# Optimization experiments

Measured on AMD Instinct MI355X. Metric: run time of the kernel, lower is better.

Reference implementation:

```python
import jax, jax.numpy as jnp
import numpy as np

TEMPERATURE = 0.5
EPS = 1e-8  # torch CosineSimilarity eps


def setup_inputs() -> dict:
    key = jax.random.key(0)
    k1, k2 = jax.random.split(key)
    N, D = 4096, 256
    z1 = jax.random.normal(k1, (N, D), dtype=jnp.float32)
    z2 = jax.random.normal(k2, (N, D), dtype=jnp.float32)
    return {"z1": z1, "z2": z2}


def reference(z1, z2):
    N = z1.shape[0]
    z = jnp.concatenate([z1, z2], axis=0)  # [2N, D]
    # cosine similarity = normalized dot products (GEMM instead of O(N^2 D) broadcast)
    norm = jnp.linalg.norm(z, axis=-1, keepdims=True)
    zn = z / jnp.maximum(norm, EPS)
    sim = (zn @ zn.T) / TEMPERATURE  # [2N, 2N]
    # mask self-similarity on the diagonal
    idx = jnp.arange(2 * N)
    sim = jnp.where(idx[:, None] == idx[None, :], -jnp.inf, sim)
    # target[i] = (i - N) mod 2N  (arange(2N).roll(N))
    target = jnp.roll(idx, N)
    logp = jax.nn.log_softmax(sim, axis=-1)
    loss = -jnp.mean(logp[idx, target])
    return loss
```

## Files before the change

kernel.cpp:

```cpp
#include <hip/hip_runtime.h>

typedef __bf16 bf16x8 __attribute__((ext_vector_type(8)));
typedef float f32x4 __attribute__((ext_vector_type(4)));

#define TWO_LOG2E 2.88539008177792681f

#define GLOADLDS16(g, l) __builtin_amdgcn_global_load_lds(                     \
    (const __attribute__((address_space(1))) void*)(g),                        \
    (__attribute__((address_space(3))) void*)(l), 16, 0, 0)

__device__ __forceinline__ unsigned f2bf(float f) {
    unsigned u = __float_as_uint(f);
    return (u + 0x7FFFu + ((u >> 16) & 1u)) >> 16;
}

__global__ void __launch_bounds__(256) normalize_kernel(
    const float* __restrict__ z1, const float* __restrict__ z2,
    unsigned short* __restrict__ zn, float* __restrict__ S, float* __restrict__ out)
{
    if (blockIdx.x < 32) S[(blockIdx.x << 8) + threadIdx.x] = 0.f;
    if (blockIdx.x == 32 && threadIdx.x == 0) out[0] = 0.f;

    const int wave = threadIdx.x >> 6, lane = threadIdx.x & 63;
    const int row = (blockIdx.x << 2) + wave;
    const float* src = (row < 4096) ? (z1 + row * 256) : (z2 + (row - 4096) * 256);
    float4 v = ((const float4*)src)[lane];
    float ss = v.x * v.x + v.y * v.y + v.z * v.z + v.w * v.w;
#pragma unroll
    for (int m = 32; m > 0; m >>= 1) ss += __shfl_xor(ss, m, 64);
    float sc = 1.0f / fmaxf(sqrtf(ss), 1e-8f);
    uint2 w;
    w.x = f2bf(v.x * sc) | (f2bf(v.y * sc) << 16);
    w.y = f2bf(v.z * sc) | (f2bf(v.w * sc) << 16);
    *(uint2*)(zn + row * 256 + (lane << 2)) = w;
}

__global__ void __launch_bounds__(512, 4) simexp_kernel(
    const unsigned short* __restrict__ zn, float* __restrict__ S)
{
    __shared__ __align__(16) unsigned short Bs[4][2048];

    const int tid = threadIdx.x;
    const int wv = tid >> 6, lane = tid & 63;
    const int q = lane >> 4, n16 = lane & 15;
    const int g = wv >> 2, wl = wv & 3;

    int ti, tj, nrep = 1;
    {
        int job = blockIdx.x;
        if (job < 496) {
            int t = 0, rem = job;
            while (rem >= 31 - t) { rem -= 31 - t; ++t; }
            ti = t; tj = t + 1 + rem;
        } else {
            ti = tj = (job - 496) << 1;
            nrep = 2;
        }
    }

    for (int rep = 0; rep < nrep; ++rep) {
        const int rT = ti + rep, cT = tj + rep;
        const bool diag = (rT == cT);
        const int colTile = cT << 8;
        const int rowW = (rT << 8) + (wv << 5);

        bf16x8 a[2][8];
#pragma unroll
        for (int rt = 0; rt < 2; ++rt)
#pragma unroll
            for (int ks = 0; ks < 8; ++ks)
                a[rt][ks] = *(const bf16x8*)(zn + ((rowW + (rt << 4) + n16) << 8)
                                                + (ks << 5) + (q << 3));

        auto stage = [&](int m) {
            const int colBase = colTile + ((m >> 2) << 5);
            const int koff = (m & 3) << 6;
            unsigned short* base = &Bs[m & 3][0];
            int s = (wl << 6) + lane;
            int c = s >> 3, d = s & 7;
            int k8 = d ^ (c & 7);
            GLOADLDS16(zn + ((colBase + c) << 8) + koff + (k8 << 3), base + (s << 3));
        };

        float rs[2][4];
#pragma unroll
        for (int i = 0; i < 2; ++i)
#pragma unroll
            for (int j = 0; j < 4; ++j) rs[i][j] = 0.f;

        f32x4 acc[2][2];
        auto consume = [&](int kc) {
            const unsigned short* bb = &Bs[kc & 3][0];
#pragma unroll
            for (int ks = 0; ks < 2; ++ks) {
                bf16x8 bf[2];
#pragma unroll
                for (int ct = 0; ct < 2; ++ct) {
                    int c  = (ct << 4) + n16;
                    int k8 = ((ks << 2) + q) ^ (c & 7);
                    bf[ct] = *(const bf16x8*)(bb + (((c << 3) + k8) << 3));
                }
#pragma unroll
                for (int rt = 0; rt < 2; ++rt)
#pragma unroll
                    for (int ct = 0; ct < 2; ++ct)
                        acc[rt][ct] = __builtin_amdgcn_mfma_f32_16x16x32_bf16(
                            a[rt][(kc << 1) + ks], bf[ct], acc[rt][ct], 0, 0, 0);
            }
        };
        auto zacc = [&]() {
#pragma unroll
            for (int rt = 0; rt < 2; ++rt)
#pragma unroll
                for (int ct = 0; ct < 2; ++ct) acc[rt][ct] = (f32x4){0.f, 0.f, 0.f, 0.f};
        };
        auto epiRC = [&](bool doCol, int ccc) {
            float cs[2] = {0.f, 0.f};
#pragma unroll
            for (int rt = 0; rt < 2; ++rt)
#pragma unroll
                for (int ct = 0; ct < 2; ++ct)
#pragma unroll
                    for (int r = 0; r < 4; ++r) {
                        float e = __builtin_amdgcn_exp2f(acc[rt][ct][r] * TWO_LOG2E);
                        rs[rt][r] += e;
                        cs[ct] += e;
                    }
            if (doCol) {
#pragma unroll
                for (int ct = 0; ct < 2; ++ct) {
                    float s = cs[ct];
                    s += __shfl_xor(s, 16, 64);
                    s += __shfl_xor(s, 32, 64);
                    if (lane < 16)
                        atomicAdd(&S[colTile + (ccc << 5) + (ct << 4) + n16], s);
                }
            }
        };

        if (g == 0) stage(0); else stage(1);

        for (int cc = 0; cc < 7; ++cc) {
            zacc();
            const bool act   = !diag || (cc >= wv);
            const bool doCol = !diag || (cc >  wv);
#pragma unroll
            for (int kc = 0; kc < 4; ++kc) {
                if ((kc & 1) == g) {
                    stage((cc << 2) + kc + 2);
                    asm volatile("s_waitcnt vmcnt(1)" ::: "memory");
                }
                __builtin_amdgcn_s_barrier();
                asm volatile("" ::: "memory");
                if (act) consume(kc);
            }
            if (act) epiRC(doCol, cc);
        }
        zacc();
        if (g == 0) { stage(30); asm volatile("s_waitcnt vmcnt(1)" ::: "memory"); }
        __builtin_amdgcn_s_barrier();
        asm volatile("" ::: "memory");
        consume(0);
        if (g == 1) { stage(31); asm volatile("s_waitcnt vmcnt(1)" ::: "memory"); }
        __builtin_amdgcn_s_barrier();
        asm volatile("" ::: "memory");
        consume(1);
        if (g == 0) { asm volatile("s_waitcnt vmcnt(0)" ::: "memory"); }
        __builtin_amdgcn_s_barrier();
        asm volatile("" ::: "memory");
        consume(2);
        if (g == 1) { asm volatile("s_waitcnt vmcnt(0)" ::: "memory"); }
        __builtin_amdgcn_s_barrier();
        asm volatile("" ::: "memory");
        consume(3);
        epiRC(!diag || (wv < 7), 7);

#pragma unroll
        for (int rt = 0; rt < 2; ++rt)
#pragma unroll
            for (int r = 0; r < 4; ++r) {
                float s = rs[rt][r];
                s += __shfl_xor(s, 1, 64);
                s += __shfl_xor(s, 2, 64);
                s += __shfl_xor(s, 4, 64);
                s += __shfl_xor(s, 8, 64);
                if (n16 == 0) atomicAdd(&S[rowW + (rt << 4) + (q << 2) + r], s);
            }
    }
}

__global__ void __launch_bounds__(256) finish_kernel(
    const unsigned short* __restrict__ zn, const float* __restrict__ S,
    float* __restrict__ out)
{
    __shared__ float vals[16];
    const int tid = threadIdx.x, lane = tid & 63, wave = tid >> 6;
    const int q = lane >> 4, n16 = lane & 15;
    const int rib = (wave << 2) + q;
    const int row = (blockIdx.x << 4) + rib;
    const int tar = (row + 4096) & 8191;

    float drr = 0.f, drt = 0.f;
#pragma unroll
    for (int i = 0; i < 4; ++i) {
        int k = (i << 6) + (n16 << 2);
        uint2 ur = *(const uint2*)(zn + (row << 8) + k);
        uint2 ut = *(const uint2*)(zn + (tar << 8) + k);
        float a0 = __uint_as_float(ur.x << 16),  a1 = __uint_as_float(ur.x & 0xFFFF0000u);
        float a2 = __uint_as_float(ur.y << 16),  a3 = __uint_as_float(ur.y & 0xFFFF0000u);
        float b0 = __uint_as_float(ut.x << 16),  b1 = __uint_as_float(ut.x & 0xFFFF0000u);
        float b2 = __uint_as_float(ut.y << 16),  b3 = __uint_as_float(ut.y & 0xFFFF0000u);
        drr += a0 * a0 + a1 * a1 + a2 * a2 + a3 * a3;
        drt += a0 * b0 + a1 * b1 + a2 * b2 + a3 * b3;
    }
#pragma unroll
    for (int m = 1; m <= 8; m <<= 1) {
        drr += __shfl_xor(drr, m, 64);
        drt += __shfl_xor(drt, m, 64);
    }
    if (n16 == 0) {
        float Sv = S[row] - __builtin_amdgcn_exp2f(drr * TWO_LOG2E);
        vals[rib] = 0.693147180559945f * __builtin_amdgcn_logf(Sv) - 2.0f * drt;
    }
    __syncthreads();
    if (tid == 0) {
        float s = 0.f;
#pragma unroll
        for (int i = 0; i < 16; ++i) s += vals[i];
        atomicAdd(out, s * (1.0f / 8192.0f));
    }
}

extern "C" void kernel_launch(void* const* d_in, const int* in_sizes, int n_in,
                              void* d_out, int out_size, void* d_ws, size_t ws_size,
                              hipStream_t stream)
{
    const float* z1 = (const float*)d_in[0];
    const float* z2 = (const float*)d_in[1];
    unsigned short* zn = (unsigned short*)d_ws;
    float* S = (float*)((char*)d_ws + 8192 * 256 * sizeof(unsigned short));
    float* out = (float*)d_out;

    normalize_kernel<<<2048, 256, 0, stream>>>(z1, z2, zn, S, out);
    simexp_kernel<<<512, 512, 0, stream>>>(zn, S);
    finish_kernel<<<512, 256, 0, stream>>>(zn, S, out);
}
```

Baseline: 110.3 us.

## Split diagonal tile jobs into direct-load path; reduce column sums via LDS

Diagonal-tile blocks now take a separate path that skips the LDS-staged pipeline and barriers. Their waves read B fragments straight from global memory and loop only over the upper-triangular chunks. Waves are paired in mirrored order across the two reps so that per-wave work balances out. Off-diagonal blocks now write per-wave column partial sums into a shared buffer and do one atomic per column after a block sync, replacing per-wave global atomics. The costs are extra LDS, a block-wide sync, and uncached global B reads on the diagonal path.

```diff
diff --git a/kernel.cpp b/kernel.cpp
--- a/kernel.cpp
+++ b/kernel.cpp
@@ -39,153 +39,230 @@
     const unsigned short* __restrict__ zn, float* __restrict__ S)
 {
     __shared__ __align__(16) unsigned short Bs[4][2048];
+    __shared__ float colpart[8][256];
 
     const int tid = threadIdx.x;
     const int wv = tid >> 6, lane = tid & 63;
     const int q = lane >> 4, n16 = lane & 15;
     const int g = wv >> 2, wl = wv & 3;
-
-    int ti, tj, nrep = 1;
-    {
-        int job = blockIdx.x;
-        if (job < 496) {
-            int t = 0, rem = job;
-            while (rem >= 31 - t) { rem -= 31 - t; ++t; }
-            ti = t; tj = t + 1 + rem;
-        } else {
-            ti = tj = (job - 496) << 1;
-            nrep = 2;
-        }
-    }
-
-    for (int rep = 0; rep < nrep; ++rep) {
-        const int rT = ti + rep, cT = tj + rep;
-        const bool diag = (rT == cT);
-        const int colTile = cT << 8;
-        const int rowW = (rT << 8) + (wv << 5);
-
-        bf16x8 a[2][8];
-#pragma unroll
-        for (int rt = 0; rt < 2; ++rt)
-#pragma unroll
-            for (int ks = 0; ks < 8; ++ks)
-                a[rt][ks] = *(const bf16x8*)(zn + ((rowW + (rt << 4) + n16) << 8)
-                                                + (ks << 5) + (q << 3));
-
-        auto stage = [&](int m) {
-            const int colBase = colTile + ((m >> 2) << 5);
-            const int koff = (m & 3) << 6;
-            unsigned short* base = &Bs[m & 3][0];
-            int s = (wl << 6) + lane;
-            int c = s >> 3, d = s & 7;
-            int k8 = d ^ (c & 7);
-            GLOADLDS16(zn + ((colBase + c) << 8) + koff + (k8 << 3), base + (s << 3));
-        };
-
-        float rs[2][4];
-#pragma unroll
-        for (int i = 0; i < 2; ++i)
-#pragma unroll
-            for (int j = 0; j < 4; ++j) rs[i][j] = 0.f;
-
-        f32x4 acc[2][2];
-        auto consume = [&](int kc) {
-            const unsigned short* bb = &Bs[kc & 3][0];
-#pragma unroll
-            for (int ks = 0; ks < 2; ++ks) {
-                bf16x8 bf[2];
-#pragma unroll
-                for (int ct = 0; ct < 2; ++ct) {
-                    int c  = (ct << 4) + n16;
-                    int k8 = ((ks << 2) + q) ^ (c & 7);
-                    bf[ct] = *(const bf16x8*)(bb + (((c << 3) + k8) << 3));
-                }
+    const int job = blockIdx.x;
+
+    if (job >= 496) {
+        const int t0 = (job - 496) << 1;
+        for (int rep = 0; rep < 2; ++rep) {
+            const int t = t0 + rep;
+            const int wp = rep ? (7 - wv) : wv;
+            const int colTile = t << 8;
+            const int rowW = colTile + (wp << 5);
+
+            bf16x8 a[2][8];
+#pragma unroll
+            for (int rt = 0; rt < 2; ++rt)
+#pragma unroll
+                for (int ks = 0; ks < 8; ++ks)
+                    a[rt][ks] = *(const bf16x8*)(zn + ((rowW + (rt << 4) + n16) << 8)
+                                                    + (ks << 5) + (q << 3));
+            float rs[2][4];
+#pragma unroll
+            for (int i = 0; i < 2; ++i)
+#pragma unroll
+                for (int j = 0; j < 4; ++j) rs[i][j] = 0.f;
+
+            for (int cc = wp; cc < 8; ++cc) {
+                f32x4 acc[2][2];
 #pragma unroll
                 for (int rt = 0; rt < 2; ++rt)
 #pragma unroll
                     for (int ct = 0; ct < 2; ++ct)
-                        acc[rt][ct] = __builtin_amdgcn_mfma_f32_16x16x32_bf16(
-                            a[rt][(kc << 1) + ks], bf[ct], acc[rt][ct], 0, 0, 0);
-            }
-        };
-        auto zacc = [&]() {
-#pragma unroll
-            for (int rt = 0; rt < 2; ++rt)
-#pragma unroll
-                for (int ct = 0; ct < 2; ++ct) acc[rt][ct] = (f32x4){0.f, 0.f, 0.f, 0.f};
-        };
-        auto epiRC = [&](bool doCol, int ccc) {
-            float cs[2] = {0.f, 0.f};
-#pragma unroll
-            for (int rt = 0; rt < 2; ++rt)
-#pragma unroll
-                for (int ct = 0; ct < 2; ++ct)
-#pragma unroll
-                    for (int r = 0; r < 4; ++r) {
-                        float e = __builtin_amdgcn_exp2f(acc[rt][ct][r] * TWO_LOG2E);
-                        rs[rt][r] += e;
-                        cs[ct] += e;
+                        acc[rt][ct] = (f32x4){0.f, 0.f, 0.f, 0.f};
+#pragma unroll
+                for (int kc = 0; kc < 4; ++kc)
+#pragma unroll
+                    for (int ks = 0; ks < 2; ++ks) {
+                        bf16x8 bf[2];
+#pragma unroll
+                        for (int ct = 0; ct < 2; ++ct) {
+                            int col = colTile + (cc << 5) + (ct << 4) + n16;
+                            bf[ct] = *(const bf16x8*)(zn + (col << 8)
+                                        + (((kc << 1) + ks) << 5) + (q << 3));
+                        }
+#pragma unroll
+                        for (int rt = 0; rt < 2; ++rt)
+#pragma unroll
+                            for (int ct = 0; ct < 2; ++ct)
+                                acc[rt][ct] = __builtin_amdgcn_mfma_f32_16x16x32_bf16(
+                                    a[rt][(kc << 1) + ks], bf[ct], acc[rt][ct], 0, 0, 0);
                     }
-            if (doCol) {
-#pragma unroll
-                for (int ct = 0; ct < 2; ++ct) {
-                    float s = cs[ct];
-                    s += __shfl_xor(s, 16, 64);
-                    s += __shfl_xor(s, 32, 64);
-                    if (lane < 16)
-                        atomicAdd(&S[colTile + (ccc << 5) + (ct << 4) + n16], s);
+                float cs[2] = {0.f, 0.f};
+#pragma unroll
+                for (int rt = 0; rt < 2; ++rt)
+#pragma unroll
+                    for (int ct = 0; ct < 2; ++ct)
+#pragma unroll
+                        for (int r = 0; r < 4; ++r) {
+                            float e = __builtin_amdgcn_exp2f(acc[rt][ct][r] * TWO_LOG2E);
+                            rs[rt][r] += e;
+                            cs[ct] += e;
+                        }
+                if (cc > wp) {
+#pragma unroll
+                    for (int ct = 0; ct < 2; ++ct) {
+                        float s = cs[ct];
+                        s += __shfl_xor(s, 16, 64);
+                        s += __shfl_xor(s, 32, 64);
+                        if (lane < 16)
+                            atomicAdd(&S[colTile + (cc << 5) + (ct << 4) + n16], s);
+                    }
                 }
             }
-        };
-
-        if (g == 0) stage(0); else stage(1);
-
-        for (int cc = 0; cc < 7; ++cc) {
-            zacc();
-            const bool act   = !diag || (cc >= wv);
-            const bool doCol = !diag || (cc >  wv);
-#pragma unroll
-            for (int kc = 0; kc < 4; ++kc) {
-                if ((kc & 1) == g) {
-                    stage((cc << 2) + kc + 2);
-                    asm volatile("s_waitcnt vmcnt(1)" ::: "memory");
+#pragma unroll
+            for (int rt = 0; rt < 2; ++rt)
+#pragma unroll
+                for (int r = 0; r < 4; ++r) {
+                    float s = rs[rt][r];
+                    s += __shfl_xor(s, 1, 64);
+                    s += __shfl_xor(s, 2, 64);
+                    s += __shfl_xor(s, 4, 64);
+                    s += __shfl_xor(s, 8, 64);
+                    if (n16 == 0) atomicAdd(&S[rowW + (rt << 4) + (q << 2) + r], s);
                 }
-                __builtin_amdgcn_s_barrier();
-                asm volatile("" ::: "memory");
-                if (act) consume(kc);
+        }
+        return;
+    }
+
+    int ti, tj;
+    {
+        int t = 0, rem = job;
+        while (rem >= 31 - t) { rem -= 31 - t; ++t; }
+        ti = t; tj = t + 1 + rem;
+    }
+    const int colTile = tj << 8;
+    const int rowW = (ti << 8) + (wv << 5);
+
+    bf16x8 a[2][8];
+#pragma unroll
+    for (int rt = 0; rt < 2; ++rt)
+#pragma unroll
+        for (int ks = 0; ks < 8; ++ks)
+            a[rt][ks] = *(const bf16x8*)(zn + ((rowW + (rt << 4) + n16) << 8)
+                                            + (ks << 5) + (q << 3));
+
+    auto stage = [&](int m) {
+        const int colBase = colTile + ((m >> 2) << 5);
+        const int koff = (m & 3) << 6;
+        unsigned short* base = &Bs[m & 3][0];
+        int s = (wl << 6) + lane;
+        int c = s >> 3, d = s & 7;
+        int k8 = d ^ (c & 7);
+        GLOADLDS16(zn + ((colBase + c) << 8) + koff + (k8 << 3), base + (s << 3));
+    };
+
+    float rs[2][4];
+#pragma unroll
+    for (int i = 0; i < 2; ++i)
+#pragma unroll
+        for (int j = 0; j < 4; ++j) rs[i][j] = 0.f;
+
+    f32x4 acc[2][2];
+    auto consume = [&](int kc) {
+        const unsigned short* bb = &Bs[kc & 3][0];
+#pragma unroll
+        for (int ks = 0; ks < 2; ++ks) {
+            bf16x8 bf[2];
+#pragma unroll
+            for (int ct = 0; ct < 2; ++ct) {
+                int c  = (ct << 4) + n16;
+                int k8 = ((ks << 2) + q) ^ (c & 7);
+                bf[ct] = *(const bf16x8*)(bb + (((c << 3) + k8) << 3));
             }
-            if (act) epiRC(doCol, cc);
-        }
+#pragma unroll
+            for (int rt = 0; rt < 2; ++rt)
+#pragma unroll
+                for (int ct = 0; ct < 2; ++ct)
+                    acc[rt][ct] = __builtin_amdgcn_mfma_f32_16x16x32_bf16(
+                        a[rt][(kc << 1) + ks], bf[ct], acc[rt][ct], 0, 0, 0);
+        }
+    };
+    auto zacc = [&]() {
+#pragma unroll
+        for (int rt = 0; rt < 2; ++rt)
+#pragma unroll
+            for (int ct = 0; ct < 2; ++ct) acc[rt][ct] = (f32x4){0.f, 0.f, 0.f, 0.f};
+    };
+    auto epiC = [&](int cc) {
+        float cs[2] = {0.f, 0.f};
+#pragma unroll
+        for (int rt = 0; rt < 2; ++rt)
+#pragma unroll
+            for (int ct = 0; ct < 2; ++ct)
+#pragma unroll
+                for (int r = 0; r < 4; ++r) {
+                    float e = __builtin_amdgcn_exp2f(acc[rt][ct][r] * TWO_LOG2E);
+                    rs[rt][r] += e;
+                    cs[ct] += e;
+                }
+#pragma unroll
+        for (int ct = 0; ct < 2; ++ct) {
+            float s = cs[ct];
+            s += __shfl_xor(s, 16, 64);
+            s += __shfl_xor(s, 32, 64);
+            if (lane < 16) colpart[wv][(cc << 5) + (ct << 4) + n16] = s;
+        }
+    };
+
+    if (g == 0) stage(0); else stage(1);
+
+    for (int cc = 0; cc < 7; ++cc) {
         zacc();
-        if (g == 0) { stage(30); asm volatile("s_waitcnt vmcnt(1)" ::: "memory"); }
-        __builtin_amdgcn_s_barrier();
-        asm volatile("" ::: "memory");
-        consume(0);
-        if (g == 1) { stage(31); asm volatile("s_waitcnt vmcnt(1)" ::: "memory"); }
-        __builtin_amdgcn_s_barrier();
-        asm volatile("" ::: "memory");
-        consume(1);
-        if (g == 0) { asm volatile("s_waitcnt vmcnt(0)" ::: "memory"); }
-        __builtin_amdgcn_s_barrier();
-        asm volatile("" ::: "memory");
-        consume(2);
-        if (g == 1) { asm volatile("s_waitcnt vmcnt(0)" ::: "memory"); }
-        __builtin_amdgcn_s_barrier();
-        asm volatile("" ::: "memory");
-        consume(3);
-        epiRC(!diag || (wv < 7), 7);
-
-#pragma unroll
-        for (int rt = 0; rt < 2; ++rt)
-#pragma unroll
-            for (int r = 0; r < 4; ++r) {
-                float s = rs[rt][r];
-                s += __shfl_xor(s, 1, 64);
-                s += __shfl_xor(s, 2, 64);
-                s += __shfl_xor(s, 4, 64);
-                s += __shfl_xor(s, 8, 64);
-                if (n16 == 0) atomicAdd(&S[rowW + (rt << 4) + (q << 2) + r], s);
+#pragma unroll
+        for (int kc = 0; kc < 4; ++kc) {
+            if ((kc & 1) == g) {
+                stage((cc << 2) + kc + 2);
+                asm volatile("s_waitcnt vmcnt(1)" ::: "memory");
             }
+            __builtin_amdgcn_s_barrier();
+            asm volatile("" ::: "memory");
+            consume(kc);
+        }
+        epiC(cc);
+    }
+    zacc();
+    if (g == 0) { stage(30); asm volatile("s_waitcnt vmcnt(1)" ::: "memory"); }
+    __builtin_amdgcn_s_barrier();
+    asm volatile("" ::: "memory");
+    consume(0);
+    if (g == 1) { stage(31); asm volatile("s_waitcnt vmcnt(1)" ::: "memory"); }
+    __builtin_amdgcn_s_barrier();
+    asm volatile("" ::: "memory");
+    consume(1);
+    if (g == 0) { asm volatile("s_waitcnt vmcnt(0)" ::: "memory"); }
+    __builtin_amdgcn_s_barrier();
+    asm volatile("" ::: "memory");
+    consume(2);
+    if (g == 1) { asm volatile("s_waitcnt vmcnt(0)" ::: "memory"); }
+    __builtin_amdgcn_s_barrier();
+    asm volatile("" ::: "memory");
+    consume(3);
+    epiC(7);
+
+#pragma unroll
+    for (int rt = 0; rt < 2; ++rt)
+#pragma unroll
+        for (int r = 0; r < 4; ++r) {
+            float s = rs[rt][r];
+            s += __shfl_xor(s, 1, 64);
+            s += __shfl_xor(s, 2, 64);
+            s += __shfl_xor(s, 4, 64);
+            s += __shfl_xor(s, 8, 64);
+            if (n16 == 0) atomicAdd(&S[rowW + (rt << 4) + (q << 2) + r], s);
+        }
+
+    __syncthreads();
+    if (tid < 256) {
+        float s = 0.f;
+#pragma unroll
+        for (int w = 0; w < 8; ++w) s += colpart[w][tid];
+        atomicAdd(&S[colTile + tid], s);
     }
 }
 
```

New measurement: 117.6 us. 1.07x slower.

## Reduce column sums in LDS and give each diagonal tile its own block

Applied to the files above, without the earlier changes.

Column exp-sums for off-diagonal tiles are now written per wave into a shared-memory buffer and combined once per block. That replaces the per-wave global atomics issued after every column chunk with one atomic per column. Diagonal tiles are now handled one per block (528 blocks instead of 512) and compute the full tile for row sums only, dropping the triangular skip logic. This cuts global atomic traffic and branching, at the cost of 8KB extra LDS, a trailing block-wide sync, and redundant MFMA work on diagonal tiles.

```diff
diff --git a/kernel.cpp b/kernel.cpp
--- a/kernel.cpp
+++ b/kernel.cpp
@@ -39,153 +39,156 @@
     const unsigned short* __restrict__ zn, float* __restrict__ S)
 {
     __shared__ __align__(16) unsigned short Bs[4][2048];
+    __shared__ float colpart[8][256];
 
     const int tid = threadIdx.x;
     const int wv = tid >> 6, lane = tid & 63;
     const int q = lane >> 4, n16 = lane & 15;
     const int g = wv >> 2, wl = wv & 3;
-
-    int ti, tj, nrep = 1;
-    {
-        int job = blockIdx.x;
-        if (job < 496) {
-            int t = 0, rem = job;
-            while (rem >= 31 - t) { rem -= 31 - t; ++t; }
-            ti = t; tj = t + 1 + rem;
-        } else {
-            ti = tj = (job - 496) << 1;
-            nrep = 2;
-        }
-    }
-
-    for (int rep = 0; rep < nrep; ++rep) {
-        const int rT = ti + rep, cT = tj + rep;
-        const bool diag = (rT == cT);
-        const int colTile = cT << 8;
-        const int rowW = (rT << 8) + (wv << 5);
-
-        bf16x8 a[2][8];
+    const int job = blockIdx.x;
+
+    int ti, tj;
+    bool diag;
+    if (job >= 496) {
+        ti = tj = job - 496;
+        diag = true;
+    } else {
+        int t = 0, rem = job;
+        while (rem >= 31 - t) { rem -= 31 - t; ++t; }
+        ti = t; tj = t + 1 + rem;
+        diag = false;
+    }
+    const int colTile = tj << 8;
+    const int rowW = (ti << 8) + (wv << 5);
+
+    bf16x8 a[2][8];
+#pragma unroll
+    for (int rt = 0; rt < 2; ++rt)
+#pragma unroll
+        for (int ks = 0; ks < 8; ++ks)
+            a[rt][ks] = *(const bf16x8*)(zn + ((rowW + (rt << 4) + n16) << 8)
+                                            + (ks << 5) + (q << 3));
+
+    auto stage = [&](int m) {
+        const int colBase = colTile + ((m >> 2) << 5);
+        const int koff = (m & 3) << 6;
+        unsigned short* base = &Bs[m & 3][0];
+        int s = (wl << 6) + lane;
+        int c = s >> 3, d = s & 7;
+        int k8 = d ^ (c & 7);
+        GLOADLDS16(zn + ((colBase + c) << 8) + koff + (k8 << 3), base + (s << 3));
+    };
+
+    float rs[2][4];
+#pragma unroll
+    for (int i = 0; i < 2; ++i)
+#pragma unroll
+        for (int j = 0; j < 4; ++j) rs[i][j] = 0.f;
+
+    f32x4 acc[2][2];
+    auto consume = [&](int kc) {
+        const unsigned short* bb = &Bs[kc & 3][0];
+#pragma unroll
+        for (int ks = 0; ks < 2; ++ks) {
+            bf16x8 bf[2];
+#pragma unroll
+            for (int ct = 0; ct < 2; ++ct) {
+                int c  = (ct << 4) + n16;
+                int k8 = ((ks << 2) + q) ^ (c & 7);
+                bf[ct] = *(const bf16x8*)(bb + (((c << 3) + k8) << 3));
+            }
+#pragma unroll
+            for (int rt = 0; rt < 2; ++rt)
+#pragma unroll
+                for (int ct = 0; ct < 2; ++ct)
+                    acc[rt][ct] = __builtin_amdgcn_mfma_f32_16x16x32_bf16(
+                        a[rt][(kc << 1) + ks], bf[ct], acc[rt][ct], 0, 0, 0);
+        }
+    };
+    auto zacc = [&]() {
 #pragma unroll
         for (int rt = 0; rt < 2; ++rt)
 #pragma unroll
-            for (int ks = 0; ks < 8; ++ks)
-                a[rt][ks] = *(const bf16x8*)(zn + ((rowW + (rt << 4) + n16) << 8)
-                                                + (ks << 5) + (q << 3));
-
-        auto stage = [&](int m) {
-            const int colBase = colTile + ((m >> 2) << 5);
-            const int koff = (m & 3) << 6;
-            unsigned short* base = &Bs[m & 3][0];
-            int s = (wl << 6) + lane;
-            int c = s >> 3, d = s & 7;
-            int k8 = d ^ (c & 7);
-            GLOADLDS16(zn + ((colBase + c) << 8) + koff + (k8 << 3), base + (s << 3));
-        };
-
-        float rs[2][4];
-#pragma unroll
-        for (int i = 0; i < 2; ++i)
-#pragma unroll
-            for (int j = 0; j < 4; ++j) rs[i][j] = 0.f;
-
-        f32x4 acc[2][2];
-        auto consume = [&](int kc) {
-            const unsigned short* bb = &Bs[kc & 3][0];
-#pragma unroll
-            for (int ks = 0; ks < 2; ++ks) {
-                bf16x8 bf[2];
-#pragma unroll
-                for (int ct = 0; ct < 2; ++ct) {
-                    int c  = (ct << 4) + n16;
-                    int k8 = ((ks << 2) + q) ^ (c & 7);
-                    bf[ct] = *(const bf16x8*)(bb + (((c << 3) + k8) << 3));
+            for (int ct = 0; ct < 2; ++ct) acc[rt][ct] = (f32x4){0.f, 0.f, 0.f, 0.f};
+    };
+    auto epiC = [&](int cc) {
+        float cs[2] = {0.f, 0.f};
+#pragma unroll
+        for (int rt = 0; rt < 2; ++rt)
+#pragma unroll
+            for (int ct = 0; ct < 2; ++ct)
+#pragma unroll
+                for (int r = 0; r < 4; ++r) {
+                    float e = __builtin_amdgcn_exp2f(acc[rt][ct][r] * TWO_LOG2E);
+                    rs[rt][r] += e;
+                    cs[ct] += e;
                 }
-#pragma unroll
-                for (int rt = 0; rt < 2; ++rt)
-#pragma unroll
-                    for (int ct = 0; ct < 2; ++ct)
-                        acc[rt][ct] = __builtin_amdgcn_mfma_f32_16x16x32_bf16(
-                            a[rt][(kc << 1) + ks], bf[ct], acc[rt][ct], 0, 0, 0);
+        if (!diag) {
+#pragma unroll
+            for (int ct = 0; ct < 2; ++ct) {
+                float s = cs[ct];
+                s += __shfl_xor(s, 16, 64);
+                s += __shfl_xor(s, 32, 64);
+                if (lane < 16) colpart[wv][(cc << 5) + (ct << 4) + n16] = s;
             }
-        };
-        auto zacc = [&]() {
-#pragma unroll
-            for (int rt = 0; rt < 2; ++rt)
-#pragma unroll
-                for (int ct = 0; ct < 2; ++ct) acc[rt][ct] = (f32x4){0.f, 0.f, 0.f, 0.f};
-        };
-        auto epiRC = [&](bool doCol, int ccc) {
-            float cs[2] = {0.f, 0.f};
-#pragma unroll
-            for (int rt = 0; rt < 2; ++rt)
-#pragma unroll
-                for (int ct = 0; ct < 2; ++ct)
-#pragma unroll
-                    for (int r = 0; r < 4; ++r) {
-                        float e = __builtin_amdgcn_exp2f(acc[rt][ct][r] * TWO_LOG2E);
-                        rs[rt][r] += e;
-                        cs[ct] += e;
-                    }
-            if (doCol) {
-#pragma unroll
-                for (int ct = 0; ct < 2; ++ct) {
-                    float s = cs[ct];
-                    s += __shfl_xor(s, 16, 64);
-                    s += __shfl_xor(s, 32, 64);
-                    if (lane < 16)
-                        atomicAdd(&S[colTile + (ccc << 5) + (ct << 4) + n16], s);
-                }
+        }
+    };
+
+    if (g == 0) stage(0); else stage(1);
+
+    for (int cc = 0; cc < 7; ++cc) {
+        zacc();
+#pragma unroll
+        for (int kc = 0; kc < 4; ++kc) {
+            if ((kc & 1) == g) {
+                stage((cc << 2) + kc + 2);
+                asm volatile("s_waitcnt vmcnt(1)" ::: "memory");
             }
-        };
-
-        if (g == 0) stage(0); else stage(1);
-
-        for (int cc = 0; cc < 7; ++cc) {
-            zacc();
-            const bool act   = !diag || (cc >= wv);
-            const bool doCol = !diag || (cc >  wv);
-#pragma unroll
-            for (int kc = 0; kc < 4; ++kc) {
-                if ((kc & 1) == g) {
-                    stage((cc << 2) + kc + 2);
-                    asm volatile("s_waitcnt vmcnt(1)" ::: "memory");
-                }
-                __builtin_amdgcn_s_barrier();
-                asm volatile("" ::: "memory");
-                if (act) consume(kc);
-            }
-            if (act) epiRC(doCol, cc);
-        }
-        zacc();
-        if (g == 0) { stage(30); asm volatile("s_waitcnt vmcnt(1)" ::: "memory"); }
-        __builtin_amdgcn_s_barrier();
-        asm volatile("" ::: "memory");
-        consume(0);
-        if (g == 1) { stage(31); asm volatile("s_waitcnt vmcnt(1)" ::: "memory"); }
-        __builtin_amdgcn_s_barrier();
-        asm volatile("" ::: "memory");
-        consume(1);
-        if (g == 0) { asm volatile("s_waitcnt vmcnt(0)" ::: "memory"); }
-        __builtin_amdgcn_s_barrier();
-        asm volatile("" ::: "memory");
-        consume(2);
-        if (g == 1) { asm volatile("s_waitcnt vmcnt(0)" ::: "memory"); }
-        __builtin_amdgcn_s_barrier();
-        asm volatile("" ::: "memory");
-        consume(3);
-        epiRC(!diag || (wv < 7), 7);
-
-#pragma unroll
-        for (int rt = 0; rt < 2; ++rt)
-#pragma unroll
-            for (int r = 0; r < 4; ++r) {
-                float s = rs[rt][r];
-                s += __shfl_xor(s, 1, 64);
-                s += __shfl_xor(s, 2, 64);
-                s += __shfl_xor(s, 4, 64);
-                s += __shfl_xor(s, 8, 64);
-                if (n16 == 0) atomicAdd(&S[rowW + (rt << 4) + (q << 2) + r], s);
-            }
+            __builtin_amdgcn_s_barrier();
+            asm volatile("" ::: "memory");
+            consume(kc);
+        }
+        epiC(cc);
+    }
+    zacc();
+    if (g == 0) { stage(30); asm volatile("s_waitcnt vmcnt(1)" ::: "memory"); }
+    __builtin_amdgcn_s_barrier();
+    asm volatile("" ::: "memory");
+    consume(0);
+    if (g == 1) { stage(31); asm volatile("s_waitcnt vmcnt(1)" ::: "memory"); }
+    __builtin_amdgcn_s_barrier();
+    asm volatile("" ::: "memory");
+    consume(1);
+    if (g == 0) { asm volatile("s_waitcnt vmcnt(0)" ::: "memory"); }
+    __builtin_amdgcn_s_barrier();
+    asm volatile("" ::: "memory");
+    consume(2);
+    if (g == 1) { asm volatile("s_waitcnt vmcnt(0)" ::: "memory"); }
+    __builtin_amdgcn_s_barrier();
+    asm volatile("" ::: "memory");
+    consume(3);
+    epiC(7);
+
+#pragma unroll
+    for (int rt = 0; rt < 2; ++rt)
+#pragma unroll
+        for (int r = 0; r < 4; ++r) {
+            float s = rs[rt][r];
+            s += __shfl_xor(s, 1, 64);
+            s += __shfl_xor(s, 2, 64);
+            s += __shfl_xor(s, 4, 64);
+            s += __shfl_xor(s, 8, 64);
+            if (n16 == 0) atomicAdd(&S[rowW + (rt << 4) + (q << 2) + r], s);
+        }
+
+    if (!diag) {
+        __syncthreads();
+        if (tid < 256) {
+            float s = 0.f;
+#pragma unroll
+            for (int w = 0; w < 8; ++w) s += colpart[w][tid];
+            atomicAdd(&S[colTile + tid], s);
+        }
     }
 }
 
@@ -242,6 +245,6 @@
     float* out = (float*)d_out;
 
     normalize_kernel<<<2048, 256, 0, stream>>>(z1, z2, zn, S, out);
-    simexp_kernel<<<512, 512, 0, stream>>>(zn, S);
+    simexp_kernel<<<528, 512, 0, stream>>>(zn, S);
     finish_kernel<<<512, 256, 0, stream>>>(zn, S, out);
 }
```

Result: faster. 101.1 us, median of 2 (-8.3%).
